# Optimization experiments

Hardware: AMD Instinct MI355X
Metric: run time of the kernel (lower is better)

## Reference

```python
import jax, jax.numpy as jnp
import numpy as np

B, N, F_IN, HID, HEADS = 4, 10000, 128, 64, 4
E = 160000
NEG_SLOPE = 0.2


def _glorot(key, shape):
    fan_in, fan_out = shape[0], shape[-1]
    lim = jnp.sqrt(6.0 / (fan_in + fan_out)).astype(jnp.float32)
    return jax.random.uniform(key, shape, jnp.float32, -lim, lim)


def setup_inputs() -> dict:
    key = jax.random.key(0)
    ks = jax.random.split(key, 10)
    x = jax.random.normal(ks[0], (B, N, F_IN), jnp.float32)
    edge_index = jax.random.randint(ks[1], (2, E), 0, N, dtype=jnp.int32)
    return {
        "x": x,
        "edge_index": edge_index,
        "W1": _glorot(ks[2], (F_IN, HEADS * HID)),
        "a_src1": _glorot(ks[3], (HEADS, HID)),
        "a_dst1": _glorot(ks[4], (HEADS, HID)),
        "b1": jnp.zeros((HID,), jnp.float32),
        "W2": _glorot(ks[5], (HID, HEADS * HID)),
        "a_src2": _glorot(ks[6], (HEADS, HID)),
        "a_dst2": _glorot(ks[7], (HEADS, HID)),
        "b2": jnp.zeros((HID,), jnp.float32),
    }


def gat_conv(x, src, dst, W, a_src, a_dst, b):
    # x: [N, F]; src/dst: [E'] (self-loops already appended)
    h = (x @ W).reshape(N, HEADS, HID)              # [N, H, C]
    al_src = jnp.einsum("nhc,hc->nh", h, a_src)      # [N, H]
    al_dst = jnp.einsum("nhc,hc->nh", h, a_dst)
    e = jax.nn.leaky_relu(al_src[src] + al_dst[dst], NEG_SLOPE)  # [E', H]
    # segment softmax over incoming edges per destination node
    m = jax.ops.segment_max(e, dst, num_segments=N)  # [N, H]
    e = jnp.exp(e - m[dst])
    s = jax.ops.segment_sum(e, dst, num_segments=N)
    alpha = e / (s[dst] + 1e-16)                     # [E', H]
    out = jax.ops.segment_sum(alpha[:, :, None] * h[src], dst, num_segments=N)  # [N, H, C]
    return out.mean(axis=1) + b                      # concat=False -> head mean


def reference(x, edge_index, W1, a_src1, a_dst1, b1, W2, a_src2, a_dst2, b2):
    loops = jnp.arange(N, dtype=edge_index.dtype)
    src = jnp.concatenate([edge_index[0], loops])
    dst = jnp.concatenate([edge_index[1], loops])

    conv1 = jax.vmap(lambda xi: gat_conv(xi, src, dst, W1, a_src1, a_dst1, b1))
    conv2 = jax.vmap(lambda xi: gat_conv(xi, src, dst, W2, a_src2, a_dst2, b2))

    h = conv1(x)                 # [B, N, HID]
    h = jax.nn.elu(h)
    h = conv2(h)
    return h
```

## Files before the change

kernel.cpp:

```cpp
#include <hip/hip_runtime.h>
#include <hip/hip_fp16.h>
#include <math.h>

#define N_NODES 10000
#define B_BATCH 4
#define F_IN_C 128
#define HID_C 64
#define HEADS_C 4
#define E_EDGES 160000
#define E_TOT (E_EDGES + N_NODES)
#define E_PAD 200000
#define NEG_SLOPE 0.2f

typedef _Float16 half8 __attribute__((ext_vector_type(8)));
typedef float f32x4 __attribute__((ext_vector_type(4)));


__device__ void wext_body(const float* __restrict__ W, const float* __restrict__ asrc,
                          const float* __restrict__ adst, __half* __restrict__ Wt,
                          int tid, int K) {
    int nc = tid / K, k = tid % K;
    float v;
    if (nc < 256) {
        v = W[k * 256 + nc];
    } else if (nc < 260) {
        int hd = nc - 256; v = 0.f;
        for (int c = 0; c < 64; c++) v += W[k * 256 + hd * 64 + c] * asrc[hd * 64 + c];
    } else if (nc < 264) {
        int hd = nc - 260; v = 0.f;
        for (int c = 0; c < 64; c++) v += W[k * 256 + hd * 64 + c] * adst[hd * 64 + c];
    } else {
        v = 0.f;
    }
    Wt[(size_t)nc * K + k] = __float2half(v);
}

__global__ void k_setup(const float* __restrict__ W1, const float* __restrict__ as1,
                        const float* __restrict__ ad1, const float* __restrict__ W2,
                        const float* __restrict__ as2, const float* __restrict__ ad2,
                        __half* __restrict__ Wt1, __half* __restrict__ Wt2,
                        int* __restrict__ deg) {
    int blk = blockIdx.x;
    if (blk < 136) {
        wext_body(W1, as1, ad1, Wt1, blk * 256 + threadIdx.x, F_IN_C);
    } else if (blk < 204) {
        wext_body(W2, as2, ad2, Wt2, (blk - 136) * 256 + threadIdx.x, HID_C);
    } else {
        int i = (blk - 204) * 256 + threadIdx.x;
        if (i < N_NODES) deg[i] = 1;
    }
}


__global__ void k_deg_count(const int* __restrict__ ei, int* __restrict__ deg) {
    int e = blockIdx.x * 256 + threadIdx.x;
    if (e < E_EDGES) atomicAdd(&deg[ei[E_EDGES + e]], 1);
}

__global__ void k_scan(const int* __restrict__ deg, int* __restrict__ offs, int* __restrict__ cursor) {
    __shared__ int lds[1024];
    int t = threadIdx.x;
    int local[10];
    int tot = 0;
#pragma unroll
    for (int j = 0; j < 10; j++) {
        int i = t * 10 + j;
        int v = (i < N_NODES) ? ((deg[i] + 3) & ~3) : 0;
        tot += v;
        local[j] = tot;
    }
    lds[t] = tot;
    __syncthreads();
    for (int ofs = 1; ofs < 1024; ofs <<= 1) {
        int v = (t >= ofs) ? lds[t - ofs] : 0;
        __syncthreads();
        lds[t] += v;
        __syncthreads();
    }
    int base = lds[t] - tot;
#pragma unroll
    for (int j = 0; j < 10; j++) {
        int i = t * 10 + j;
        if (i < N_NODES) {
            offs[i + 1] = base + local[j];
            cursor[i] = (j == 0) ? base : base + local[j - 1];
        }
    }
    if (t == 0) offs[0] = 0;
}

__global__ void k_scatter(const int* __restrict__ ei, int* __restrict__ cursor,
                          int* __restrict__ csr_b, int* __restrict__ csr_dst) {
    int e = blockIdx.x * 256 + threadIdx.x;
    if (e < E_TOT) {
        int s, d;
        if (e < E_EDGES) { s = ei[e]; d = ei[E_EDGES + e]; }
        else { s = d = e - E_EDGES; }
        int pos = atomicAdd(&cursor[d], 1);
        csr_b[pos] = s << 7;
        csr_dst[pos] = d;
    }
}

__global__ void k_pad(const int* __restrict__ cursor, const int* __restrict__ offs,
                      int* __restrict__ csr_b, int* __restrict__ csr_dst) {
    int tid = blockIdx.x * 256 + threadIdx.x;
    if (tid >= N_NODES * 4) return;
    int d = tid >> 2, ps = tid & 3;
    int pos = cursor[d] + ps;
    if (pos < offs[d + 1]) { csr_b[pos] = 0; csr_dst[pos] = -1; }
}


template <int K, typename XT>
__launch_bounds__(256)
__global__ void k_gemm(const XT* __restrict__ x, const __half* __restrict__ Wt,
                       __half* __restrict__ h2, float* __restrict__ alsrc, float* __restrict__ aldst) {
    int t = threadIdx.x;
    int w = t >> 6, lane = t & 63;
    int b = blockIdx.y;
    int node0 = blockIdx.x * 16;
    int col = lane & 15, kblk = lane >> 4;

    const XT* xr = x + ((size_t)b * N_NODES + node0 + col) * K + kblk * 8;

    f32x4 acc0 = {0.f, 0.f, 0.f, 0.f};
    f32x4 acc1 = {0.f, 0.f, 0.f, 0.f};
    f32x4 acc2 = {0.f, 0.f, 0.f, 0.f};
    f32x4 acc3 = {0.f, 0.f, 0.f, 0.f};
    f32x4 accal = {0.f, 0.f, 0.f, 0.f};

#pragma unroll
    for (int k0 = 0; k0 < K; k0 += 32) {
        half8 a;
        if constexpr (sizeof(XT) == 4) {
            float4 xa = *(const float4*)(xr + k0);
            float4 xc = *(const float4*)(xr + k0 + 4);
            a[0] = (_Float16)xa.x; a[1] = (_Float16)xa.y; a[2] = (_Float16)xa.z; a[3] = (_Float16)xa.w;
            a[4] = (_Float16)xc.x; a[5] = (_Float16)xc.y; a[6] = (_Float16)xc.z; a[7] = (_Float16)xc.w;
        } else {
            a = *(const half8*)(xr + k0);
        }
        const __half* wtk = Wt + kblk * 8 + k0;
        half8 b0 = *(const half8*)(wtk + (size_t)((w * 4 + 0) * 16 + col) * K);
        half8 b1 = *(const half8*)(wtk + (size_t)((w * 4 + 1) * 16 + col) * K);
        half8 b2 = *(const half8*)(wtk + (size_t)((w * 4 + 2) * 16 + col) * K);
        half8 b3 = *(const half8*)(wtk + (size_t)((w * 4 + 3) * 16 + col) * K);
        acc0 = __builtin_amdgcn_mfma_f32_16x16x32_f16(a, b0, acc0, 0, 0, 0);
        acc1 = __builtin_amdgcn_mfma_f32_16x16x32_f16(a, b1, acc1, 0, 0, 0);
        acc2 = __builtin_amdgcn_mfma_f32_16x16x32_f16(a, b2, acc2, 0, 0, 0);
        acc3 = __builtin_amdgcn_mfma_f32_16x16x32_f16(a, b3, acc3, 0, 0, 0);
        if (w == 0) {
            half8 bal = *(const half8*)(wtk + (size_t)(256 + col) * K);
            accal = __builtin_amdgcn_mfma_f32_16x16x32_f16(a, bal, accal, 0, 0, 0);
        }
    }

    {
        __half* dst = h2 + ((size_t)(b * 4 + w) * N_NODES + node0 + kblk * 4) * 64 + col;
#pragma unroll
        for (int r = 0; r < 4; r++) dst[(size_t)r * 64 + 0 * 16] = __float2half(acc0[r]);
#pragma unroll
        for (int r = 0; r < 4; r++) dst[(size_t)r * 64 + 1 * 16] = __float2half(acc1[r]);
#pragma unroll
        for (int r = 0; r < 4; r++) dst[(size_t)r * 64 + 2 * 16] = __float2half(acc2[r]);
#pragma unroll
        for (int r = 0; r < 4; r++) dst[(size_t)r * 64 + 3 * 16] = __float2half(acc3[r]);
    }
    if (w == 0 && col < 8) {
        int node = node0 + kblk * 4;
        size_t nb = (size_t)b * N_NODES;
        if (col < 4) {
            float* d = alsrc + (nb + node) * 4 + col;
#pragma unroll
            for (int r = 0; r < 4; r++) d[r * 4] = accal[r];
        } else {
            float* d = aldst + (nb + node) * 4 + (col - 4);
#pragma unroll
            for (int r = 0; r < 4; r++) d[r * 4] = accal[r];
        }
    }
}


__launch_bounds__(256)
__global__ void k_alpha(const float* __restrict__ alsrc, const float* __restrict__ aldst,
                        const int* __restrict__ csr_b, const int* __restrict__ csr_dst,
                        const int* __restrict__ offs, float* __restrict__ alpha) {
    int j = blockIdx.x * 256 + threadIdx.x;
    int e_act = offs[N_NODES];
    if (j >= e_act) return;
    int b = blockIdx.y;
    size_t base = (size_t)b * 4 * E_PAD + j;
    int dst = csr_dst[j];
    if (dst < 0) {
        alpha[base] = 0.f;
        alpha[base + E_PAD] = 0.f;
        alpha[base + (size_t)2 * E_PAD] = 0.f;
        alpha[base + (size_t)3 * E_PAD] = 0.f;
        return;
    }
    int src4 = csr_b[j] >> 5;
    const float* als = alsrc + (size_t)b * N_NODES * 4;
    float4 s4 = *(const float4*)(als + src4);
    float4 d4 = *(const float4*)(aldst + ((size_t)b * N_NODES + dst) * 4);
    float a;
    a = s4.x + d4.x; a = a > 0.f ? a : NEG_SLOPE * a; float e0 = __expf(a);
    a = s4.y + d4.y; a = a > 0.f ? a : NEG_SLOPE * a; float e1 = __expf(a);
    a = s4.z + d4.z; a = a > 0.f ? a : NEG_SLOPE * a; float e2 = __expf(a);
    a = s4.w + d4.w; a = a > 0.f ? a : NEG_SLOPE * a; float e3 = __expf(a);
    alpha[base] = e0;
    alpha[base + E_PAD] = e1;
    alpha[base + (size_t)2 * E_PAD] = e2;
    alpha[base + (size_t)3 * E_PAD] = e3;
}


#define QUAD_FMA16(p4, g0, g1, g2, g3)                                                    \
    {                                                                                     \
        float2 f01, f23;                                                                  \
        f01 = __half22float2(*(__half2*)&g0.x); f23 = __half22float2(*(__half2*)&g0.y);   \
        acc.x += p4.x * f01.x; acc.y += p4.x * f01.y; acc.z += p4.x * f23.x; acc.w += p4.x * f23.y; \
        f01 = __half22float2(*(__half2*)&g1.x); f23 = __half22float2(*(__half2*)&g1.y);   \
        acc.x += p4.y * f01.x; acc.y += p4.y * f01.y; acc.z += p4.y * f23.x; acc.w += p4.y * f23.y; \
        f01 = __half22float2(*(__half2*)&g2.x); f23 = __half22float2(*(__half2*)&g2.y);   \
        acc.x += p4.z * f01.x; acc.y += p4.z * f01.y; acc.z += p4.z * f23.x; acc.w += p4.z * f23.y; \
        f01 = __half22float2(*(__half2*)&g3.x); f23 = __half22float2(*(__half2*)&g3.y);   \
        acc.x += p4.w * f01.x; acc.y += p4.w * f01.y; acc.z += p4.w * f23.x; acc.w += p4.w * f23.y; \
        sacc += p4.x + p4.y + p4.z + p4.w;                                                \
    }

template <bool LAYER1>
__launch_bounds__(256)
__global__ void k_agg(const __half* __restrict__ h2, const float* __restrict__ alpha,
                      const int* __restrict__ offs, const int* __restrict__ csr_b,
                      const float* __restrict__ bias, void* __restrict__ outv) {
    int t = threadIdx.x;
    int bid = blockIdx.x;
    int xcd = bid & 7;
    int b = xcd >> 1;
    int local = (bid >> 3) * 2 + (xcd & 1);
    int wv = t >> 6, lane = t & 63;
    int hd = lane >> 4, cl = lane & 15;
    int dst = local * 4 + wv;

    const char* hcb = (const char*)(h2 + (size_t)(b * 4 + hd) * N_NODES * 64);
    const float* ec = alpha + (size_t)(b * 4 + hd) * E_PAD;
    int s0 = offs[dst], s1 = offs[dst + 1];
    int cl8 = cl * 8;

    float4 acc = make_float4(0.f, 0.f, 0.f, 0.f);
    float sacc = 0.f;
    int4 c_cur = *(const int4*)(csr_b + s0);
    float4 p_cur = *(const float4*)(ec + s0);
    uint2 g0 = *(const uint2*)(hcb + (unsigned)(c_cur.x + cl8));
    uint2 g1 = *(const uint2*)(hcb + (unsigned)(c_cur.y + cl8));
    uint2 g2 = *(const uint2*)(hcb + (unsigned)(c_cur.z + cl8));
    uint2 g3 = *(const uint2*)(hcb + (unsigned)(c_cur.w + cl8));
    int jn = (s0 + 4 < s1) ? s0 + 4 : s0;
    int4 c_nxt = *(const int4*)(csr_b + jn);
    float4 p_nxt = *(const float4*)(ec + jn);

    for (int j = s0 + 4; j < s1; j += 4) {
        uint2 m0 = *(const uint2*)(hcb + (unsigned)(c_nxt.x + cl8));
        uint2 m1 = *(const uint2*)(hcb + (unsigned)(c_nxt.y + cl8));
        uint2 m2 = *(const uint2*)(hcb + (unsigned)(c_nxt.z + cl8));
        uint2 m3 = *(const uint2*)(hcb + (unsigned)(c_nxt.w + cl8));
        int j2 = (j + 4 < s1) ? j + 4 : j;
        int4 c_tmp = *(const int4*)(csr_b + j2);
        float4 p_tmp = *(const float4*)(ec + j2);
        QUAD_FMA16(p_cur, g0, g1, g2, g3)
        g0 = m0; g1 = m1; g2 = m2; g3 = m3;
        p_cur = p_nxt;
        c_nxt = c_tmp; p_nxt = p_tmp;
    }
    QUAD_FMA16(p_cur, g0, g1, g2, g3)

    float inv = 1.f / (sacc + 1e-16f);
    float4 v = make_float4(acc.x * inv, acc.y * inv, acc.z * inv, acc.w * inv);
#pragma unroll
    for (int o = 16; o < 64; o <<= 1) {
        v.x += __shfl_xor(v.x, o);
        v.y += __shfl_xor(v.y, o);
        v.z += __shfl_xor(v.z, o);
        v.w += __shfl_xor(v.w, o);
    }
    if (lane < 16) {
        float4 b4 = *(const float4*)(bias + cl * 4);
        float ox = v.x * 0.25f + b4.x;
        float oy = v.y * 0.25f + b4.y;
        float oz = v.z * 0.25f + b4.z;
        float ow = v.w * 0.25f + b4.w;
        if (LAYER1) {
            ox = ox > 0.f ? ox : expm1f(ox);
            oy = oy > 0.f ? oy : expm1f(oy);
            oz = oz > 0.f ? oz : expm1f(oz);
            ow = ow > 0.f ? ow : expm1f(ow);
            __half2 lo = __floats2half2_rn(ox, oy);
            __half2 hi = __floats2half2_rn(oz, ow);
            uint2 pk = make_uint2(*(unsigned*)&lo, *(unsigned*)&hi);
            *(uint2*)((__half*)outv + ((size_t)b * N_NODES + dst) * 64 + cl * 4) = pk;
        } else {
            *(float4*)((float*)outv + ((size_t)b * N_NODES + dst) * 64 + cl * 4) =
                make_float4(ox, oy, oz, ow);
        }
    }
}


extern "C" void kernel_launch(void* const* d_in, const int* in_sizes, int n_in,
                              void* d_out, int out_size, void* d_ws, size_t ws_size,
                              hipStream_t stream) {
    const float* x = (const float*)d_in[0];
    const int* ei = (const int*)d_in[1];
    const float* W1 = (const float*)d_in[2];
    const float* as1 = (const float*)d_in[3];
    const float* ad1 = (const float*)d_in[4];
    const float* b1 = (const float*)d_in[5];
    const float* W2 = (const float*)d_in[6];
    const float* as2 = (const float*)d_in[7];
    const float* ad2 = (const float*)d_in[8];
    const float* b2 = (const float*)d_in[9];
    float* out = (float*)d_out;

    char* p = (char*)d_ws;
    int* deg = (int*)p;            p += sizeof(int) * N_NODES;
    int* offs = (int*)p;           p += sizeof(int) * (N_NODES + 4);
    int* cursor = (int*)p;         p += sizeof(int) * N_NODES;
    int* csr_b = (int*)p;          p += sizeof(int) * E_PAD;
    int* csr_dst = (int*)p;        p += sizeof(int) * E_PAD;
    __half* Wt1 = (__half*)p;      p += sizeof(__half) * 272 * F_IN_C;
    __half* Wt2 = (__half*)p;      p += sizeof(__half) * 272 * HID_C;
    float* alsrc = (float*)p;      p += sizeof(float) * B_BATCH * N_NODES * 4;
    float* aldst = (float*)p;      p += sizeof(float) * B_BATCH * N_NODES * 4;
    __half* h2 = (__half*)p;       p += sizeof(__half) * (size_t)B_BATCH * N_NODES * 256;
    __half* x2 = (__half*)p;       p += sizeof(__half) * (size_t)B_BATCH * N_NODES * 64;
    p = (char*)(((size_t)p + 15) & ~(size_t)15);
    float* alpha = (float*)p;      p += sizeof(float) * (size_t)B_BATCH * 4 * E_PAD;

    k_setup<<<244, 256, 0, stream>>>(W1, as1, ad1, W2, as2, ad2, Wt1, Wt2, deg);

    k_deg_count<<<(E_EDGES + 255) / 256, 256, 0, stream>>>(ei, deg);
    k_scan<<<1, 1024, 0, stream>>>(deg, offs, cursor);
    k_scatter<<<(E_TOT + 255) / 256, 256, 0, stream>>>(ei, cursor, csr_b, csr_dst);
    k_pad<<<(N_NODES * 4 + 255) / 256, 256, 0, stream>>>(cursor, offs, csr_b, csr_dst);

    dim3 gGemm(N_NODES / 16, B_BATCH);
    dim3 gAlpha((E_PAD + 255) / 256, B_BATCH);
    int gAgg = B_BATCH * 2500;

    k_gemm<F_IN_C, float><<<gGemm, 256, 0, stream>>>(x, Wt1, h2, alsrc, aldst);
    k_alpha<<<gAlpha, 256, 0, stream>>>(alsrc, aldst, csr_b, csr_dst, offs, alpha);
    k_agg<true><<<gAgg, 256, 0, stream>>>(h2, alpha, offs, csr_b, b1, x2);

    k_gemm<HID_C, __half><<<gGemm, 256, 0, stream>>>(x2, Wt2, h2, alsrc, aldst);
    k_alpha<<<gAlpha, 256, 0, stream>>>(alsrc, aldst, csr_b, csr_dst, offs, alpha);
    k_agg<false><<<gAgg, 256, 0, stream>>>(h2, alpha, offs, csr_b, b2, out);
}
```

Baseline: 207.6 us.

## Interleave heads in node-major h layout and pad CSR to eight edges

The GEMM now writes h as node-major with all four heads contiguous (256 halves per node) instead of head-major planes, so each gathered source row covers all heads in one 512-byte span. CSR segments are padded to multiples of 8 and the aggregation loop handles 8 edges per iteration with doubled prefetch, giving more memory-level parallelism per wave. The cost is extra padding edges (larger alpha and CSR buffers, more zero-weight work for low-degree nodes) and higher register pressure in the aggregation kernel.

```diff
diff --git a/kernel.cpp b/kernel.cpp
--- a/kernel.cpp
+++ b/kernel.cpp
@@ -9,7 +9,7 @@
 #define HEADS_C 4
 #define E_EDGES 160000
 #define E_TOT (E_EDGES + N_NODES)
-#define E_PAD 200000
+#define E_OCT 240000
 #define NEG_SLOPE 0.2f
 
 typedef _Float16 half8 __attribute__((ext_vector_type(8)));
@@ -65,7 +65,7 @@
 #pragma unroll
     for (int j = 0; j < 10; j++) {
         int i = t * 10 + j;
-        int v = (i < N_NODES) ? ((deg[i] + 3) & ~3) : 0;
+        int v = (i < N_NODES) ? ((deg[i] + 7) & ~7) : 0;
         tot += v;
         local[j] = tot;
     }
@@ -97,7 +97,7 @@
         if (e < E_EDGES) { s = ei[e]; d = ei[E_EDGES + e]; }
         else { s = d = e - E_EDGES; }
         int pos = atomicAdd(&cursor[d], 1);
-        csr_b[pos] = s << 7;
+        csr_b[pos] = s << 9;
         csr_dst[pos] = d;
     }
 }
@@ -105,8 +105,8 @@
 __global__ void k_pad(const int* __restrict__ cursor, const int* __restrict__ offs,
                       int* __restrict__ csr_b, int* __restrict__ csr_dst) {
     int tid = blockIdx.x * 256 + threadIdx.x;
-    if (tid >= N_NODES * 4) return;
-    int d = tid >> 2, ps = tid & 3;
+    if (tid >= N_NODES * 8) return;
+    int d = tid >> 3, ps = tid & 7;
     int pos = cursor[d] + ps;
     if (pos < offs[d + 1]) { csr_b[pos] = 0; csr_dst[pos] = -1; }
 }
@@ -157,15 +157,15 @@
     }
 
     {
-        __half* dst = h2 + ((size_t)(b * 4 + w) * N_NODES + node0 + kblk * 4) * 64 + col;
-#pragma unroll
-        for (int r = 0; r < 4; r++) dst[(size_t)r * 64 + 0 * 16] = __float2half(acc0[r]);
-#pragma unroll
-        for (int r = 0; r < 4; r++) dst[(size_t)r * 64 + 1 * 16] = __float2half(acc1[r]);
-#pragma unroll
-        for (int r = 0; r < 4; r++) dst[(size_t)r * 64 + 2 * 16] = __float2half(acc2[r]);
-#pragma unroll
-        for (int r = 0; r < 4; r++) dst[(size_t)r * 64 + 3 * 16] = __float2half(acc3[r]);
+        __half* dst = h2 + ((size_t)b * N_NODES + node0 + kblk * 4) * 256 + w * 64 + col;
+#pragma unroll
+        for (int r = 0; r < 4; r++) dst[(size_t)r * 256 + 0 * 16] = __float2half(acc0[r]);
+#pragma unroll
+        for (int r = 0; r < 4; r++) dst[(size_t)r * 256 + 1 * 16] = __float2half(acc1[r]);
+#pragma unroll
+        for (int r = 0; r < 4; r++) dst[(size_t)r * 256 + 2 * 16] = __float2half(acc2[r]);
+#pragma unroll
+        for (int r = 0; r < 4; r++) dst[(size_t)r * 256 + 3 * 16] = __float2half(acc3[r]);
     }
     if (w == 0 && col < 8) {
         int node = node0 + kblk * 4;
@@ -191,16 +191,16 @@
     int e_act = offs[N_NODES];
     if (j >= e_act) return;
     int b = blockIdx.y;
-    size_t base = (size_t)b * 4 * E_PAD + j;
+    size_t base = (size_t)b * 4 * E_OCT + j;
     int dst = csr_dst[j];
     if (dst < 0) {
         alpha[base] = 0.f;
-        alpha[base + E_PAD] = 0.f;
-        alpha[base + (size_t)2 * E_PAD] = 0.f;
-        alpha[base + (size_t)3 * E_PAD] = 0.f;
+        alpha[base + E_OCT] = 0.f;
+        alpha[base + (size_t)2 * E_OCT] = 0.f;
+        alpha[base + (size_t)3 * E_OCT] = 0.f;
         return;
     }
-    int src4 = csr_b[j] >> 5;
+    int src4 = csr_b[j] >> 7;
     const float* als = alsrc + (size_t)b * N_NODES * 4;
     float4 s4 = *(const float4*)(als + src4);
     float4 d4 = *(const float4*)(aldst + ((size_t)b * N_NODES + dst) * 4);
@@ -210,9 +210,9 @@
     a = s4.z + d4.z; a = a > 0.f ? a : NEG_SLOPE * a; float e2 = __expf(a);
     a = s4.w + d4.w; a = a > 0.f ? a : NEG_SLOPE * a; float e3 = __expf(a);
     alpha[base] = e0;
-    alpha[base + E_PAD] = e1;
-    alpha[base + (size_t)2 * E_PAD] = e2;
-    alpha[base + (size_t)3 * E_PAD] = e3;
+    alpha[base + E_OCT] = e1;
+    alpha[base + (size_t)2 * E_OCT] = e2;
+    alpha[base + (size_t)3 * E_OCT] = e3;
 }
 
 
@@ -244,37 +244,54 @@
     int hd = lane >> 4, cl = lane & 15;
     int dst = local * 4 + wv;
 
-    const char* hcb = (const char*)(h2 + (size_t)(b * 4 + hd) * N_NODES * 64);
-    const float* ec = alpha + (size_t)(b * 4 + hd) * E_PAD;
+    const char* hcb = (const char*)(h2 + (size_t)b * N_NODES * 256);
+    const float* ec = alpha + (size_t)(b * 4 + hd) * E_OCT;
     int s0 = offs[dst], s1 = offs[dst + 1];
-    int cl8 = cl * 8;
+    int laneoff = (hd << 7) | (cl << 3);
 
     float4 acc = make_float4(0.f, 0.f, 0.f, 0.f);
     float sacc = 0.f;
-    int4 c_cur = *(const int4*)(csr_b + s0);
-    float4 p_cur = *(const float4*)(ec + s0);
-    uint2 g0 = *(const uint2*)(hcb + (unsigned)(c_cur.x + cl8));
-    uint2 g1 = *(const uint2*)(hcb + (unsigned)(c_cur.y + cl8));
-    uint2 g2 = *(const uint2*)(hcb + (unsigned)(c_cur.z + cl8));
-    uint2 g3 = *(const uint2*)(hcb + (unsigned)(c_cur.w + cl8));
-    int jn = (s0 + 4 < s1) ? s0 + 4 : s0;
-    int4 c_nxt = *(const int4*)(csr_b + jn);
-    float4 p_nxt = *(const float4*)(ec + jn);
-
-    for (int j = s0 + 4; j < s1; j += 4) {
-        uint2 m0 = *(const uint2*)(hcb + (unsigned)(c_nxt.x + cl8));
-        uint2 m1 = *(const uint2*)(hcb + (unsigned)(c_nxt.y + cl8));
-        uint2 m2 = *(const uint2*)(hcb + (unsigned)(c_nxt.z + cl8));
-        uint2 m3 = *(const uint2*)(hcb + (unsigned)(c_nxt.w + cl8));
-        int j2 = (j + 4 < s1) ? j + 4 : j;
-        int4 c_tmp = *(const int4*)(csr_b + j2);
-        float4 p_tmp = *(const float4*)(ec + j2);
-        QUAD_FMA16(p_cur, g0, g1, g2, g3)
+    int4 cA = *(const int4*)(csr_b + s0);
+    int4 cB = *(const int4*)(csr_b + s0 + 4);
+    float4 pA = *(const float4*)(ec + s0);
+    float4 pB = *(const float4*)(ec + s0 + 4);
+    uint2 g0 = *(const uint2*)(hcb + (unsigned)(cA.x + laneoff));
+    uint2 g1 = *(const uint2*)(hcb + (unsigned)(cA.y + laneoff));
+    uint2 g2 = *(const uint2*)(hcb + (unsigned)(cA.z + laneoff));
+    uint2 g3 = *(const uint2*)(hcb + (unsigned)(cA.w + laneoff));
+    uint2 g4 = *(const uint2*)(hcb + (unsigned)(cB.x + laneoff));
+    uint2 g5 = *(const uint2*)(hcb + (unsigned)(cB.y + laneoff));
+    uint2 g6 = *(const uint2*)(hcb + (unsigned)(cB.z + laneoff));
+    uint2 g7 = *(const uint2*)(hcb + (unsigned)(cB.w + laneoff));
+    int jn = (s0 + 8 < s1) ? s0 + 8 : s0;
+    int4 cA2 = *(const int4*)(csr_b + jn);
+    int4 cB2 = *(const int4*)(csr_b + jn + 4);
+    float4 pA2 = *(const float4*)(ec + jn);
+    float4 pB2 = *(const float4*)(ec + jn + 4);
+
+    for (int j = s0 + 8; j < s1; j += 8) {
+        uint2 m0 = *(const uint2*)(hcb + (unsigned)(cA2.x + laneoff));
+        uint2 m1 = *(const uint2*)(hcb + (unsigned)(cA2.y + laneoff));
+        uint2 m2 = *(const uint2*)(hcb + (unsigned)(cA2.z + laneoff));
+        uint2 m3 = *(const uint2*)(hcb + (unsigned)(cA2.w + laneoff));
+        uint2 m4 = *(const uint2*)(hcb + (unsigned)(cB2.x + laneoff));
+        uint2 m5 = *(const uint2*)(hcb + (unsigned)(cB2.y + laneoff));
+        uint2 m6 = *(const uint2*)(hcb + (unsigned)(cB2.z + laneoff));
+        uint2 m7 = *(const uint2*)(hcb + (unsigned)(cB2.w + laneoff));
+        int j2 = (j + 8 < s1) ? j + 8 : j;
+        int4 cA3 = *(const int4*)(csr_b + j2);
+        int4 cB3 = *(const int4*)(csr_b + j2 + 4);
+        float4 pA3 = *(const float4*)(ec + j2);
+        float4 pB3 = *(const float4*)(ec + j2 + 4);
+        QUAD_FMA16(pA, g0, g1, g2, g3)
+        QUAD_FMA16(pB, g4, g5, g6, g7)
         g0 = m0; g1 = m1; g2 = m2; g3 = m3;
-        p_cur = p_nxt;
-        c_nxt = c_tmp; p_nxt = p_tmp;
-    }
-    QUAD_FMA16(p_cur, g0, g1, g2, g3)
+        g4 = m4; g5 = m5; g6 = m6; g7 = m7;
+        pA = pA2; pB = pB2;
+        cA2 = cA3; cB2 = cB3; pA2 = pA3; pB2 = pB3;
+    }
+    QUAD_FMA16(pA, g0, g1, g2, g3)
+    QUAD_FMA16(pB, g4, g5, g6, g7)
 
     float inv = 1.f / (sacc + 1e-16f);
     float4 v = make_float4(acc.x * inv, acc.y * inv, acc.z * inv, acc.w * inv);
@@ -327,8 +344,8 @@
     int* deg = (int*)p;            p += sizeof(int) * N_NODES;
     int* offs = (int*)p;           p += sizeof(int) * (N_NODES + 4);
     int* cursor = (int*)p;         p += sizeof(int) * N_NODES;
-    int* csr_b = (int*)p;          p += sizeof(int) * E_PAD;
-    int* csr_dst = (int*)p;        p += sizeof(int) * E_PAD;
+    int* csr_b = (int*)p;          p += sizeof(int) * E_OCT;
+    int* csr_dst = (int*)p;        p += sizeof(int) * E_OCT;
     __half* Wt1 = (__half*)p;      p += sizeof(__half) * 272 * F_IN_C;
     __half* Wt2 = (__half*)p;      p += sizeof(__half) * 272 * HID_C;
     float* alsrc = (float*)p;      p += sizeof(float) * B_BATCH * N_NODES * 4;
@@ -336,17 +353,17 @@
     __half* h2 = (__half*)p;       p += sizeof(__half) * (size_t)B_BATCH * N_NODES * 256;
     __half* x2 = (__half*)p;       p += sizeof(__half) * (size_t)B_BATCH * N_NODES * 64;
     p = (char*)(((size_t)p + 15) & ~(size_t)15);
-    float* alpha = (float*)p;      p += sizeof(float) * (size_t)B_BATCH * 4 * E_PAD;
+    float* alpha = (float*)p;      p += sizeof(float) * (size_t)B_BATCH * 4 * E_OCT;
 
     k_setup<<<244, 256, 0, stream>>>(W1, as1, ad1, W2, as2, ad2, Wt1, Wt2, deg);
 
     k_deg_count<<<(E_EDGES + 255) / 256, 256, 0, stream>>>(ei, deg);
     k_scan<<<1, 1024, 0, stream>>>(deg, offs, cursor);
     k_scatter<<<(E_TOT + 255) / 256, 256, 0, stream>>>(ei, cursor, csr_b, csr_dst);
-    k_pad<<<(N_NODES * 4 + 255) / 256, 256, 0, stream>>>(cursor, offs, csr_b, csr_dst);
+    k_pad<<<(N_NODES * 8 + 255) / 256, 256, 0, stream>>>(cursor, offs, csr_b, csr_dst);
 
     dim3 gGemm(N_NODES / 16, B_BATCH);
-    dim3 gAlpha((E_PAD + 255) / 256, B_BATCH);
+    dim3 gAlpha((E_OCT + 255) / 256, B_BATCH);
     int gAgg = B_BATCH * 2500;
 
     k_gemm<F_IN_C, float><<<gGemm, 256, 0, stream>>>(x, Wt1, h2, alsrc, aldst);
```

New measurement: 204.8 us. About the same (-1.4%).
